# Kernel optimization log

Measured on AMD Instinct MI355X. Metric: run time of the kernel, lower is better.

Reference implementation:

```python
import jax, jax.numpy as jnp
import numpy as np

SCALE = 64.0  # quantization scale: float -> signed 8-bit index
PAD = 1
K = 3


def setup_inputs() -> dict:
    key = jax.random.key(0)
    k1, k2, k3 = jax.random.split(key, 3)
    x = jax.random.normal(k1, (8, 64, 32, 32), dtype=jnp.float32)
    weight = jax.random.normal(k2, (64, 64, 3, 3), dtype=jnp.float32) * 0.1
    bias = jax.random.normal(k3, (64,), dtype=jnp.float32)
    # 256x256 approximate-multiplier LUT: dequantized exact product perturbed by a
    # deterministic relative error, emulating an MBM approximate multiplier table.
    q = (np.arange(256, dtype=np.float64) - 128.0) / SCALE
    exact = np.outer(q, q)
    rng = np.random.default_rng(0)
    lut = (exact * (1.0 + 0.02 * rng.standard_normal((256, 256)))).astype(np.float32)
    return {"x": x, "weight": weight, "bias": bias, "lut": jnp.asarray(lut)}


def reference(x, weight, bias, lut):
    B, C, H, W = x.shape
    O = weight.shape[0]
    oh = (H + 2 * PAD - K) + 1
    ow = (W + 2 * PAD - K) + 1
    L = oh * ow
    P = C * K * K

    xp = jnp.pad(x, ((0, 0), (0, 0), (PAD, PAD), (PAD, PAD)))
    # im2col: [B, C*K*K, oh, ow], feature dim ordered channel-slowest (matches
    # torch unfold(2,k).unfold(3,k).reshape ordering intent)
    patches = jax.lax.conv_general_dilated_patches(xp, (K, K), (1, 1), 'VALID')
    patches = patches.reshape(B, P, L)

    # quantize both operands to 8-bit LUT indices in [0, 255]
    qx = jnp.clip(jnp.round(patches * SCALE), -128, 127).astype(jnp.int32) + 128  # [B,P,L]
    qw = jnp.clip(jnp.round(weight.reshape(O, P) * SCALE), -128, 127).astype(jnp.int32) + 128  # [O,P]

    lut_flat = lut.reshape(-1)
    base = qx * 256  # row offsets, loop-invariant  [B,P,L]

    def body(carry, wrow):  # wrow: [P] indices for one output channel
        prod = jnp.take(lut_flat, base + wrow[None, :, None], axis=0)  # [B,P,L]
        return carry, prod.sum(axis=1)  # [B,L]

    _, out = jax.lax.scan(body, 0.0, qw)  # [O,B,L]
    out = out.transpose(1, 0, 2).reshape(B, O, oh, ow)
    return out + bias[None, :, None, None]
```

## Files before the change

kernel.cpp:

```cpp
#include <hip/hip_runtime.h>
#include <hip/hip_fp16.h>


#define NT 256

__device__ __forceinline__ int quantize(float v) {
    int q = (int)rintf(v * 64.0f);
    q = q < -128 ? -128 : q;
    q = q > 127 ? 127 : q;
    return q + 128;
}

__device__ __forceinline__ void gll16(const void* g, void* l) {
    __builtin_amdgcn_global_load_lds(
        (const __attribute__((address_space(1))) unsigned int*)g,
        (__attribute__((address_space(3))) unsigned int*)l, 16, 0, 0);
}

__global__ __launch_bounds__(NT, 2)
void build_T4(const float* __restrict__ w, const float* __restrict__ lut,
              unsigned int* __restrict__ T)
{
    __shared__ float band[8 * 257];
    __shared__ unsigned char qw4[4][576];

    const int tid = threadIdx.x;
    const int quad = blockIdx.x >> 5;
    const int q0 = (blockIdx.x & 31) << 3;

    for (int i = tid; i < 4 * 576; i += NT) {
        int oo = i / 576, idx = i - oo * 576;
        qw4[oo][idx] = (unsigned char)quantize(w[(quad * 4 + oo) * 576 + idx]);
    }
    for (int i = tid; i < 8 * 256; i += NT) {
        int r = i >> 8, c2 = i & 255;
        band[r * 257 + c2] = lut[(q0 + r) * 256 + c2];
    }
    __syncthreads();

    for (int it = 0; it < 6; ++it) {
        int idx = it * NT + tid;
        int c = idx / 24;
        int rem = idx - c * 24;
        int ky = rem >> 3;
        int qxl = rem & 7;
        const float* brow = band + qxl * 257;
        const int wb = c * 9 + ky * 3;
        unsigned int* dst =
            T + (((size_t)(quad * 64 + c) * 3 + ky) * 256 + q0 + qxl) * 6;
        #pragma unroll
        for (int k = 0; k < 3; ++k) {
            unsigned int h0 = __half_as_ushort(__float2half(brow[qw4[0][wb + k]]));
            unsigned int h1 = __half_as_ushort(__float2half(brow[qw4[1][wb + k]]));
            unsigned int h2 = __half_as_ushort(__float2half(brow[qw4[2][wb + k]]));
            unsigned int h3 = __half_as_ushort(__float2half(brow[qw4[3][wb + k]]));
            *(uint2*)(dst + k * 2) = make_uint2(h0 | (h1 << 16), h2 | (h3 << 16));
        }
    }
}

__global__ __launch_bounds__(NT, 2)
void approx_main(const float* __restrict__ x, const unsigned int* __restrict__ T,
                 const float* __restrict__ bias, float* __restrict__ out)
{
    __shared__ __align__(16) unsigned char Ts[36864];
    __shared__ unsigned int plane[2][2][100];

    const int tid = threadIdx.x;
    const int bid = blockIdx.x;
    const int quad = bid & 15;
    const int g = bid >> 4;
    const int b = g >> 2;
    const int qt = g & 3;

    const int p = tid >> 7;
    const int lt = tid & 127;
    const int yl = lt >> 4;
    const int x0 = (lt & 15) << 1;
    const int yg = qt * 8 + yl;

    const char* Tg = (const char*)T + (size_t)quad * 1179648;
    const float* xb = x + (size_t)b * 65536;

    for (int i = tid; i < 400; i += NT) ((unsigned int*)plane)[i] = 0x80808080u;

    int hvalid = 0, hrow = 0, hpr = 0;
    float xh = 0.f;
    if (lt < 64) {
        int hr = lt >> 5;
        int grow = qt * 8 + (hr ? 8 : -1);
        hvalid = (grow >= 0 && grow < 32);
        hrow = grow;
        hpr = hr ? 9 : 0;
        if (hvalid) xh = xb[p * 1024 + hrow * 32 + (lt & 31)];
    }
    float2 xv = *(const float2*)(xb + p * 1024 + yg * 32 + x0);

    __syncthreads();

    __half2 z2 = __float2half2_rn(0.f);
    __half2 ah00 = z2, ah01 = z2, ah10 = z2, ah11 = z2;
    float a32[2][4] = {{0.f, 0.f, 0.f, 0.f}, {0.f, 0.f, 0.f, 0.f}};

    for (int t = 0; t < 32; ++t) {
        const int buf = t & 1;
        unsigned char* pb = (unsigned char*)plane[p][buf];
        int qa = quantize(xv.x), qb = quantize(xv.y);
        *(unsigned short*)(pb + (yl + 1) * 40 + 4 + x0) =
            (unsigned short)(qa | (qb << 8));
        if (lt < 64 && hvalid) pb[hpr * 40 + 4 + (lt & 31)] = (unsigned char)quantize(xh);

        {
            const char* src = Tg + (size_t)t * 36864 + tid * 16;
            char* dst = (char*)Ts + tid * 16;
            #pragma unroll
            for (int k = 0; k < 9; ++k) gll16(src + k * 4096, dst + k * 4096);
        }
        if (t < 31) {
            const int cn = 2 * (t + 1) + p;
            xv = *(const float2*)(xb + cn * 1024 + yg * 32 + x0);
            if (lt < 64 && hvalid) xh = xb[cn * 1024 + hrow * 32 + (lt & 31)];
        }
        __syncthreads();

        const unsigned int* pl = plane[p][buf];
        const char* Tp = (const char*)Ts + p * 18432;
        #pragma unroll
        for (int ky = 0; ky < 3; ++ky) {
            const int pbase = (yl + ky) * 10;
            const int j0 = (x0 + 3) >> 2;
            unsigned int wlo = pl[pbase + j0];
            unsigned int whi = pl[pbase + j0 + 1];
            unsigned long long dv = ((unsigned long long)whi << 32) | wlo;
            unsigned int qbts = (unsigned int)(dv >> (((x0 + 3) & 3) * 8));
            int m0 = (int)(qbts & 255u), m1 = (int)((qbts >> 8) & 255u);
            int m2 = (int)((qbts >> 16) & 255u), m3 = (int)(qbts >> 24);
            const char* Tk = Tp + ky * 6144;
            uint2 A = *(const uint2*)(Tk + m0 * 24);
            uint2 Bv = *(const uint2*)(Tk + m1 * 24 + 8);
            uint2 Cv = *(const uint2*)(Tk + m2 * 24 + 16);
            uint2 D = *(const uint2*)(Tk + m1 * 24);
            uint2 E = *(const uint2*)(Tk + m2 * 24 + 8);
            uint2 F = *(const uint2*)(Tk + m3 * 24 + 16);
            ah00 = __hadd2(ah00, *(__half2*)&A.x);  ah01 = __hadd2(ah01, *(__half2*)&A.y);
            ah00 = __hadd2(ah00, *(__half2*)&Bv.x); ah01 = __hadd2(ah01, *(__half2*)&Bv.y);
            ah00 = __hadd2(ah00, *(__half2*)&Cv.x); ah01 = __hadd2(ah01, *(__half2*)&Cv.y);
            ah10 = __hadd2(ah10, *(__half2*)&D.x);  ah11 = __hadd2(ah11, *(__half2*)&D.y);
            ah10 = __hadd2(ah10, *(__half2*)&E.x);  ah11 = __hadd2(ah11, *(__half2*)&E.y);
            ah10 = __hadd2(ah10, *(__half2*)&F.x);  ah11 = __hadd2(ah11, *(__half2*)&F.y);
        }
        if (t & 1) {
            a32[0][0] += __low2float(ah00); a32[0][1] += __high2float(ah00);
            a32[0][2] += __low2float(ah01); a32[0][3] += __high2float(ah01);
            a32[1][0] += __low2float(ah10); a32[1][1] += __high2float(ah10);
            a32[1][2] += __low2float(ah11); a32[1][3] += __high2float(ah11);
            ah00 = z2; ah01 = z2; ah10 = z2; ah11 = z2;
        }
        __syncthreads();
    }

    float* red = (float*)Ts;
    if (p) {
        #pragma unroll
        for (int px = 0; px < 2; ++px)
            #pragma unroll
            for (int oo = 0; oo < 4; ++oo)
                red[lt * 8 + px * 4 + oo] = a32[px][oo];
    }
    __syncthreads();
    if (!p) {
        const int o0 = quad * 4;
        #pragma unroll
        for (int oo = 0; oo < 4; ++oo) {
            float bo = bias[o0 + oo];
            float2 r;
            r.x = a32[0][oo] + red[lt * 8 + oo]     + bo;
            r.y = a32[1][oo] + red[lt * 8 + 4 + oo] + bo;
            *(float2*)(out + ((size_t)b * 64 + o0 + oo) * 1024 + yg * 32 + x0) = r;
        }
    }
}

#define BW1 61
__global__ __launch_bounds__(NT, 2)
void approxconv2d_v1(const float* __restrict__ x,
                     const float* __restrict__ w,
                     const float* __restrict__ bias,
                     const float* __restrict__ lut,
                     float* __restrict__ out)
{
    __shared__ float band[256 * BW1];
    __shared__ unsigned int plane[340];
    __shared__ unsigned char qwrow[576];
    __shared__ int s_min;

    const int tid = threadIdx.x;
    const int bid = blockIdx.x;
    const int b = bid >> 6;
    const int o = bid & 63;

    if (tid == 0) s_min = 255;
    for (int i = tid; i < 340; i += NT) plane[i] = 0x80808080u;
    __syncthreads();

    int lmin = 255;
    for (int i = tid; i < 576; i += NT) {
        int q = quantize(w[o * 576 + i]);
        qwrow[i] = (unsigned char)q;
        lmin = lmin < q ? lmin : q;
    }
    atomicMin(&s_min, lmin);
    __syncthreads();

    int cmin = s_min;
    if (cmin > 256 - BW1) cmin = 256 - BW1;

    for (int i = tid; i < 256 * BW1; i += NT) {
        int qx = i / BW1;
        int cc = i - qx * BW1;
        band[i] = lut[(qx << 8) + cmin + cc];
    }

    const int y  = tid >> 3;
    const int xq = tid & 7;
    const int x0 = xq << 2;

    float acc0 = 0.f, acc1 = 0.f, acc2 = 0.f, acc3 = 0.f;
    const float* xb = x + (size_t)b * 64 * 1024;
    unsigned char* pb = (unsigned char*)plane;

    for (int c = 0; c < 64; ++c) {
        __syncthreads();
        float4 xv = *(const float4*)(xb + c * 1024 + y * 32 + x0);
        int qa = quantize(xv.x), qb = quantize(xv.y);
        int qc = quantize(xv.z), qd = quantize(xv.w);
        int wbase = (y + 1) * 40 + x0 + 1;
        pb[wbase + 0] = (unsigned char)qa;
        pb[wbase + 1] = (unsigned char)qb;
        pb[wbase + 2] = (unsigned char)qc;
        pb[wbase + 3] = (unsigned char)qd;
        __syncthreads();

        const unsigned char* qwp = qwrow + c * 9;
        #pragma unroll
        for (int ky = 0; ky < 3; ++ky) {
            int ro = (y + ky) * 10 + xq;
            unsigned int r0 = plane[ro];
            unsigned int r1 = plane[ro + 1];
            int ee[6];
            ee[0] = (int)(r0 & 255u);
            ee[1] = (int)((r0 >> 8) & 255u);
            ee[2] = (int)((r0 >> 16) & 255u);
            ee[3] = (int)(r0 >> 24);
            ee[4] = (int)(r1 & 255u);
            ee[5] = (int)((r1 >> 8) & 255u);
            int pp[6];
            #pragma unroll
            for (int tt = 0; tt < 6; ++tt) pp[tt] = ee[tt] * BW1;
            #pragma unroll
            for (int kx = 0; kx < 3; ++kx) {
                int cq = (int)qwp[ky * 3 + kx];
                int cc = cq - cmin;
                if ((unsigned)cc < (unsigned)BW1) {
                    acc0 += band[pp[kx + 0] + cc];
                    acc1 += band[pp[kx + 1] + cc];
                    acc2 += band[pp[kx + 2] + cc];
                    acc3 += band[pp[kx + 3] + cc];
                } else {
                    acc0 += lut[(ee[kx + 0] << 8) + cq];
                    acc1 += lut[(ee[kx + 1] << 8) + cq];
                    acc2 += lut[(ee[kx + 2] << 8) + cq];
                    acc3 += lut[(ee[kx + 3] << 8) + cq];
                }
            }
        }
    }

    float bo = bias[o];
    float4 r;
    r.x = acc0 + bo; r.y = acc1 + bo; r.z = acc2 + bo; r.w = acc3 + bo;
    *(float4*)(out + (size_t)bid * 1024 + y * 32 + x0) = r;
}

extern "C" void kernel_launch(void* const* d_in, const int* in_sizes, int n_in,
                              void* d_out, int out_size, void* d_ws, size_t ws_size,
                              hipStream_t stream) {
    const float* x    = (const float*)d_in[0];
    const float* wgt  = (const float*)d_in[1];
    const float* bias = (const float*)d_in[2];
    const float* lut  = (const float*)d_in[3];
    float* out = (float*)d_out;

    const size_t T_BYTES = (size_t)16 * 64 * 3 * 256 * 24;
    if (ws_size >= T_BYTES) {
        hipLaunchKernelGGL(build_T4, dim3(512), dim3(NT), 0, stream,
                           wgt, lut, (unsigned int*)d_ws);
        hipLaunchKernelGGL(approx_main, dim3(512), dim3(NT), 0, stream,
                           x, (const unsigned int*)d_ws, bias, out);
    } else {
        hipLaunchKernelGGL(approxconv2d_v1, dim3(512), dim3(NT), 0, stream,
                           x, wgt, bias, lut, out);
    }
}
```

Baseline: 56.39 us.

## Keep 4-channel table slice resident in LDS and split-K over channels with atomics

The main kernel now gives each block a fixed group of 4 input channels for 4 output channels and a 16-row half image. It loads that 72 KB table slice into LDS once, then loops over the 8 batch images instead of streaming the whole per-channel table every iteration. Partial sums go to the output through float atomic adds, and a new bias_init kernel pre-fills the output with bias. This removes repeated table reloads and per-iteration global-to-LDS traffic. In exchange it adds an extra launch, many atomic operations, and larger LDS use that may lower occupancy, and summation order is no longer deterministic.

```diff
diff --git a/kernel.cpp b/kernel.cpp
--- a/kernel.cpp
+++ b/kernel.cpp
@@ -15,6 +15,14 @@
     __builtin_amdgcn_global_load_lds(
         (const __attribute__((address_space(1))) unsigned int*)g,
         (__attribute__((address_space(3))) unsigned int*)l, 16, 0, 0);
+}
+
+__global__ __launch_bounds__(NT, 4)
+void bias_init(const float* __restrict__ bias, float* __restrict__ out)
+{
+    int v = blockIdx.x * NT + threadIdx.x;
+    float bo = bias[(v >> 8) & 63];
+    ((float4*)out)[v] = make_float4(bo, bo, bo, bo);
 }
 
 __global__ __launch_bounds__(NT, 2)
@@ -60,124 +68,124 @@
 }
 
 __global__ __launch_bounds__(NT, 2)
-void approx_main(const float* __restrict__ x, const unsigned int* __restrict__ T,
-                 const float* __restrict__ bias, float* __restrict__ out)
+void approx_res(const float* __restrict__ x, const unsigned int* __restrict__ T,
+                float* __restrict__ out)
 {
-    __shared__ __align__(16) unsigned char Ts[36864];
-    __shared__ unsigned int plane[2][2][100];
+    __shared__ __align__(16) unsigned char Tq[73728];
+    __shared__ __align__(8) unsigned char planes[4][720];
 
     const int tid = threadIdx.x;
     const int bid = blockIdx.x;
     const int quad = bid & 15;
-    const int g = bid >> 4;
-    const int b = g >> 2;
-    const int qt = g & 3;
-
-    const int p = tid >> 7;
-    const int lt = tid & 127;
-    const int yl = lt >> 4;
-    const int x0 = (lt & 15) << 1;
-    const int yg = qt * 8 + yl;
-
-    const char* Tg = (const char*)T + (size_t)quad * 1179648;
-    const float* xb = x + (size_t)b * 65536;
-
-    for (int i = tid; i < 400; i += NT) ((unsigned int*)plane)[i] = 0x80808080u;
-
-    int hvalid = 0, hrow = 0, hpr = 0;
+    const int g2 = bid >> 4;
+    const int cg = g2 & 15;
+    const int h = g2 >> 4;
+    const int c0 = cg * 4;
+    const int o0 = quad * 4;
+
+    const int yl = tid >> 4;
+    const int x0 = (tid & 15) << 1;
+    const int yg = h * 16 + yl;
+
+    {
+        const char* Tg = (const char*)T + (size_t)(quad * 64 + c0) * 18432;
+        #pragma unroll
+        for (int p2 = 0; p2 < 18; ++p2)
+            gll16(Tg + p2 * 4096 + tid * 16, (char*)Tq + p2 * 4096 + tid * 16);
+    }
+    for (int i = tid; i < 720; i += NT) ((unsigned int*)planes)[i] = 0x80808080u;
+
+    const int hc = tid >> 6;
+    const int hr = (tid >> 5) & 1;
+    const int hcol = tid & 31;
+    const int hgrow = h * 16 + (hr ? 16 : -1);
+    const int hvalid = (hgrow >= 0 && hgrow < 32);
+    const int hpr = hr ? 17 : 0;
+
+    float2 xv[4];
     float xh = 0.f;
-    if (lt < 64) {
-        int hr = lt >> 5;
-        int grow = qt * 8 + (hr ? 8 : -1);
-        hvalid = (grow >= 0 && grow < 32);
-        hrow = grow;
-        hpr = hr ? 9 : 0;
-        if (hvalid) xh = xb[p * 1024 + hrow * 32 + (lt & 31)];
-    }
-    float2 xv = *(const float2*)(xb + p * 1024 + yg * 32 + x0);
+    {
+        const float* xb = x;
+        #pragma unroll
+        for (int c = 0; c < 4; ++c)
+            xv[c] = *(const float2*)(xb + (size_t)(c0 + c) * 1024 + yg * 32 + x0);
+        if (hvalid) xh = xb[(size_t)(c0 + hc) * 1024 + hgrow * 32 + hcol];
+    }
 
     __syncthreads();
 
-    __half2 z2 = __float2half2_rn(0.f);
-    __half2 ah00 = z2, ah01 = z2, ah10 = z2, ah11 = z2;
-    float a32[2][4] = {{0.f, 0.f, 0.f, 0.f}, {0.f, 0.f, 0.f, 0.f}};
-
-    for (int t = 0; t < 32; ++t) {
-        const int buf = t & 1;
-        unsigned char* pb = (unsigned char*)plane[p][buf];
-        int qa = quantize(xv.x), qb = quantize(xv.y);
-        *(unsigned short*)(pb + (yl + 1) * 40 + 4 + x0) =
-            (unsigned short)(qa | (qb << 8));
-        if (lt < 64 && hvalid) pb[hpr * 40 + 4 + (lt & 31)] = (unsigned char)quantize(xh);
+    float a32[2][4];
+    #pragma unroll
+    for (int px = 0; px < 2; ++px)
+        #pragma unroll
+        for (int oo = 0; oo < 4; ++oo) a32[px][oo] = 0.f;
+
+    for (int b = 0; b < 8; ++b) {
+        #pragma unroll
+        for (int c = 0; c < 4; ++c) {
+            int qa = quantize(xv[c].x), qb = quantize(xv[c].y);
+            *(unsigned short*)(&planes[c][(yl + 1) * 40 + 4 + x0]) =
+                (unsigned short)(qa | (qb << 8));
+        }
+        if (hvalid) planes[hc][hpr * 40 + 4 + hcol] = (unsigned char)quantize(xh);
+        __syncthreads();
 
         {
-            const char* src = Tg + (size_t)t * 36864 + tid * 16;
-            char* dst = (char*)Ts + tid * 16;
+            const int bn = b < 7 ? b + 1 : 7;
+            const float* xb = x + (size_t)bn * 65536;
             #pragma unroll
-            for (int k = 0; k < 9; ++k) gll16(src + k * 4096, dst + k * 4096);
-        }
-        if (t < 31) {
-            const int cn = 2 * (t + 1) + p;
-            xv = *(const float2*)(xb + cn * 1024 + yg * 32 + x0);
-            if (lt < 64 && hvalid) xh = xb[cn * 1024 + hrow * 32 + (lt & 31)];
+            for (int c = 0; c < 4; ++c)
+                xv[c] = *(const float2*)(xb + (size_t)(c0 + c) * 1024 + yg * 32 + x0);
+            if (hvalid) xh = xb[(size_t)(c0 + hc) * 1024 + hgrow * 32 + hcol];
+        }
+
+        __half2 z2 = __float2half2_rn(0.f);
+        __half2 ah00 = z2, ah01 = z2, ah10 = z2, ah11 = z2;
+        #pragma unroll
+        for (int c = 0; c < 4; ++c) {
+            const unsigned int* pl = (const unsigned int*)planes[c];
+            const char* Tc = (const char*)Tq + c * 18432;
+            #pragma unroll
+            for (int ky = 0; ky < 3; ++ky) {
+                const int pbase = (yl + ky) * 10;
+                const int j0 = (x0 + 3) >> 2;
+                unsigned int wlo = pl[pbase + j0];
+                unsigned int whi = pl[pbase + j0 + 1];
+                unsigned long long dv = ((unsigned long long)whi << 32) | wlo;
+                unsigned int qbts = (unsigned int)(dv >> (((x0 + 3) & 3) * 8));
+                int m0 = (int)(qbts & 255u), m1 = (int)((qbts >> 8) & 255u);
+                int m2 = (int)((qbts >> 16) & 255u), m3 = (int)(qbts >> 24);
+                const char* Tk = Tc + ky * 6144;
+                uint2 A = *(const uint2*)(Tk + m0 * 24);
+                uint2 Bv = *(const uint2*)(Tk + m1 * 24 + 8);
+                uint2 Cv = *(const uint2*)(Tk + m2 * 24 + 16);
+                uint2 D = *(const uint2*)(Tk + m1 * 24);
+                uint2 E = *(const uint2*)(Tk + m2 * 24 + 8);
+                uint2 F = *(const uint2*)(Tk + m3 * 24 + 16);
+                ah00 = __hadd2(ah00, *(__half2*)&A.x);  ah01 = __hadd2(ah01, *(__half2*)&A.y);
+                ah00 = __hadd2(ah00, *(__half2*)&Bv.x); ah01 = __hadd2(ah01, *(__half2*)&Bv.y);
+                ah00 = __hadd2(ah00, *(__half2*)&Cv.x); ah01 = __hadd2(ah01, *(__half2*)&Cv.y);
+                ah10 = __hadd2(ah10, *(__half2*)&D.x);  ah11 = __hadd2(ah11, *(__half2*)&D.y);
+                ah10 = __hadd2(ah10, *(__half2*)&E.x);  ah11 = __hadd2(ah11, *(__half2*)&E.y);
+                ah10 = __hadd2(ah10, *(__half2*)&F.x);  ah11 = __hadd2(ah11, *(__half2*)&F.y);
+            }
+            if (c & 1) {
+                a32[0][0] += __low2float(ah00); a32[0][1] += __high2float(ah00);
+                a32[0][2] += __low2float(ah01); a32[0][3] += __high2float(ah01);
+                a32[1][0] += __low2float(ah10); a32[1][1] += __high2float(ah10);
+                a32[1][2] += __low2float(ah11); a32[1][3] += __high2float(ah11);
+                ah00 = z2; ah01 = z2; ah10 = z2; ah11 = z2;
+            }
+        }
+
+        #pragma unroll
+        for (int oo = 0; oo < 4; ++oo) {
+            float* p = out + ((size_t)(b * 64 + o0 + oo)) * 1024 + yg * 32 + x0;
+            unsafeAtomicAdd(p,     a32[0][oo]);
+            unsafeAtomicAdd(p + 1, a32[1][oo]);
+            a32[0][oo] = 0.f; a32[1][oo] = 0.f;
         }
         __syncthreads();
-
-        const unsigned int* pl = plane[p][buf];
-        const char* Tp = (const char*)Ts + p * 18432;
-        #pragma unroll
-        for (int ky = 0; ky < 3; ++ky) {
-            const int pbase = (yl + ky) * 10;
-            const int j0 = (x0 + 3) >> 2;
-            unsigned int wlo = pl[pbase + j0];
-            unsigned int whi = pl[pbase + j0 + 1];
-            unsigned long long dv = ((unsigned long long)whi << 32) | wlo;
-            unsigned int qbts = (unsigned int)(dv >> (((x0 + 3) & 3) * 8));
-            int m0 = (int)(qbts & 255u), m1 = (int)((qbts >> 8) & 255u);
-            int m2 = (int)((qbts >> 16) & 255u), m3 = (int)(qbts >> 24);
-            const char* Tk = Tp + ky * 6144;
-            uint2 A = *(const uint2*)(Tk + m0 * 24);
-            uint2 Bv = *(const uint2*)(Tk + m1 * 24 + 8);
-            uint2 Cv = *(const uint2*)(Tk + m2 * 24 + 16);
-            uint2 D = *(const uint2*)(Tk + m1 * 24);
-            uint2 E = *(const uint2*)(Tk + m2 * 24 + 8);
-            uint2 F = *(const uint2*)(Tk + m3 * 24 + 16);
-            ah00 = __hadd2(ah00, *(__half2*)&A.x);  ah01 = __hadd2(ah01, *(__half2*)&A.y);
-            ah00 = __hadd2(ah00, *(__half2*)&Bv.x); ah01 = __hadd2(ah01, *(__half2*)&Bv.y);
-            ah00 = __hadd2(ah00, *(__half2*)&Cv.x); ah01 = __hadd2(ah01, *(__half2*)&Cv.y);
-            ah10 = __hadd2(ah10, *(__half2*)&D.x);  ah11 = __hadd2(ah11, *(__half2*)&D.y);
-            ah10 = __hadd2(ah10, *(__half2*)&E.x);  ah11 = __hadd2(ah11, *(__half2*)&E.y);
-            ah10 = __hadd2(ah10, *(__half2*)&F.x);  ah11 = __hadd2(ah11, *(__half2*)&F.y);
-        }
-        if (t & 1) {
-            a32[0][0] += __low2float(ah00); a32[0][1] += __high2float(ah00);
-            a32[0][2] += __low2float(ah01); a32[0][3] += __high2float(ah01);
-            a32[1][0] += __low2float(ah10); a32[1][1] += __high2float(ah10);
-            a32[1][2] += __low2float(ah11); a32[1][3] += __high2float(ah11);
-            ah00 = z2; ah01 = z2; ah10 = z2; ah11 = z2;
-        }
-        __syncthreads();
-    }
-
-    float* red = (float*)Ts;
-    if (p) {
-        #pragma unroll
-        for (int px = 0; px < 2; ++px)
-            #pragma unroll
-            for (int oo = 0; oo < 4; ++oo)
-                red[lt * 8 + px * 4 + oo] = a32[px][oo];
-    }
-    __syncthreads();
-    if (!p) {
-        const int o0 = quad * 4;
-        #pragma unroll
-        for (int oo = 0; oo < 4; ++oo) {
-            float bo = bias[o0 + oo];
-            float2 r;
-            r.x = a32[0][oo] + red[lt * 8 + oo]     + bo;
-            r.y = a32[1][oo] + red[lt * 8 + 4 + oo] + bo;
-            *(float2*)(out + ((size_t)b * 64 + o0 + oo) * 1024 + yg * 32 + x0) = r;
-        }
     }
 }
 
@@ -293,10 +301,11 @@
 
     const size_t T_BYTES = (size_t)16 * 64 * 3 * 256 * 24;
     if (ws_size >= T_BYTES) {
+        hipLaunchKernelGGL(bias_init, dim3(512), dim3(NT), 0, stream, bias, out);
         hipLaunchKernelGGL(build_T4, dim3(512), dim3(NT), 0, stream,
                            wgt, lut, (unsigned int*)d_ws);
-        hipLaunchKernelGGL(approx_main, dim3(512), dim3(NT), 0, stream,
-                           x, (const unsigned int*)d_ws, bias, out);
+        hipLaunchKernelGGL(approx_res, dim3(512), dim3(NT), 0, stream,
+                           x, (const unsigned int*)d_ws, out);
     } else {
         hipLaunchKernelGGL(approxconv2d_v1, dim3(512), dim3(NT), 0, stream,
                            x, wgt, bias, lut, out);
```

Result: slower. 92.89 us (+64.7%).

## Double-buffer LUT slab in LDS and overlap next-slice loads with compute

Applied to the files above, without the earlier changes.

Adds a second LDS buffer for the per-channel-pair LUT slab and issues global_load_lds for slice t+1 before computing slice t. Hand-written s_waitcnt vmcnt/barrier sequences replace __syncthreads so that only the previous iteration's loads are waited on. This hides global-to-LDS latency behind the LUT gather/accumulate work. In exchange it doubles LDS use, which may reduce occupancy, and it depends on an exact count of outstanding vector memory ops.

```diff
diff --git a/kernel.cpp b/kernel.cpp
--- a/kernel.cpp
+++ b/kernel.cpp
@@ -63,7 +63,7 @@
 void approx_main(const float* __restrict__ x, const unsigned int* __restrict__ T,
                  const float* __restrict__ bias, float* __restrict__ out)
 {
-    __shared__ __align__(16) unsigned char Ts[36864];
+    __shared__ __align__(16) unsigned char Ts[2][36864];
     __shared__ unsigned int plane[2][2][100];
 
     const int tid = threadIdx.x;
@@ -84,47 +84,51 @@
 
     for (int i = tid; i < 400; i += NT) ((unsigned int*)plane)[i] = 0x80808080u;
 
-    int hvalid = 0, hrow = 0, hpr = 0;
-    float xh = 0.f;
-    if (lt < 64) {
-        int hr = lt >> 5;
-        int grow = qt * 8 + (hr ? 8 : -1);
-        hvalid = (grow >= 0 && grow < 32);
-        hrow = grow;
-        hpr = hr ? 9 : 0;
-        if (hvalid) xh = xb[p * 1024 + hrow * 32 + (lt & 31)];
-    }
+    const int hr = (lt >> 5) & 1;
+    const int hgrow = qt * 8 + (hr ? 8 : -1);
+    const int hvalid = (hgrow >= 0 && hgrow < 32);
+    const int hrow = hgrow < 0 ? 0 : (hgrow > 31 ? 31 : hgrow);
+    const int hpr = hr ? 9 : 0;
+    const int hcol = lt & 31;
+
     float2 xv = *(const float2*)(xb + p * 1024 + yg * 32 + x0);
-
+    float xh = xb[p * 1024 + hrow * 32 + hcol];
+    {
+        const char* src = Tg + tid * 16;
+        char* dst = (char*)Ts[0] + tid * 16;
+        #pragma unroll
+        for (int k = 0; k < 9; ++k) gll16(src + k * 4096, dst + k * 4096);
+    }
     __syncthreads();
 
     __half2 z2 = __float2half2_rn(0.f);
     __half2 ah00 = z2, ah01 = z2, ah10 = z2, ah11 = z2;
     float a32[2][4] = {{0.f, 0.f, 0.f, 0.f}, {0.f, 0.f, 0.f, 0.f}};
 
+    #pragma unroll 1
     for (int t = 0; t < 32; ++t) {
         const int buf = t & 1;
         unsigned char* pb = (unsigned char*)plane[p][buf];
         int qa = quantize(xv.x), qb = quantize(xv.y);
         *(unsigned short*)(pb + (yl + 1) * 40 + 4 + x0) =
             (unsigned short)(qa | (qb << 8));
-        if (lt < 64 && hvalid) pb[hpr * 40 + 4 + (lt & 31)] = (unsigned char)quantize(xh);
+        if (lt < 64 && hvalid) pb[hpr * 40 + 4 + hcol] = (unsigned char)quantize(xh);
 
         {
-            const char* src = Tg + (size_t)t * 36864 + tid * 16;
-            char* dst = (char*)Ts + tid * 16;
+            const int tn = t < 31 ? t + 1 : 31;
+            const int cn = 2 * tn + p;
+            xv = *(const float2*)(xb + cn * 1024 + yg * 32 + x0);
+            xh = xb[cn * 1024 + hrow * 32 + hcol];
+            const char* src = Tg + (size_t)tn * 36864 + tid * 16;
+            char* dst = (char*)Ts[buf ^ 1] + tid * 16;
             #pragma unroll
             for (int k = 0; k < 9; ++k) gll16(src + k * 4096, dst + k * 4096);
         }
-        if (t < 31) {
-            const int cn = 2 * (t + 1) + p;
-            xv = *(const float2*)(xb + cn * 1024 + yg * 32 + x0);
-            if (lt < 64 && hvalid) xh = xb[cn * 1024 + hrow * 32 + (lt & 31)];
-        }
-        __syncthreads();
+
+        asm volatile("s_waitcnt vmcnt(11) lgkmcnt(0)\n\ts_barrier" ::: "memory");
 
         const unsigned int* pl = plane[p][buf];
-        const char* Tp = (const char*)Ts + p * 18432;
+        const char* Tp = (const char*)Ts[buf] + p * 18432;
         #pragma unroll
         for (int ky = 0; ky < 3; ++ky) {
             const int pbase = (yl + ky) * 10;
@@ -156,10 +160,13 @@
             a32[1][2] += __low2float(ah11); a32[1][3] += __high2float(ah11);
             ah00 = z2; ah01 = z2; ah10 = z2; ah11 = z2;
         }
-        __syncthreads();
-    }
-
-    float* red = (float*)Ts;
+
+        asm volatile("s_waitcnt lgkmcnt(0)\n\ts_barrier" ::: "memory");
+    }
+
+    __syncthreads();
+
+    float* red = (float*)Ts[0];
     if (p) {
         #pragma unroll
         for (int px = 0; px < 2; ++px)
```

Measured after the change: 55.56 us. Within noise of the previous version (-1.5%).
